# Optimization experiments

Hardware: AMD Instinct MI355X
Metric: run time of the kernel (lower is better)

The kernel has to match this reference:

```python
import jax, jax.numpy as jnp
import numpy as np

N_SAMPLE = 256
POS_IOU_THRESH = 0.7
NEG_IOU_THRESH = 0.3
POS_RATIO = 0.5


def _bbox_iou(bbox_a, bbox_b):
    # bbox_a: [K,4], bbox_b: [G,4] in (x1,y1,x2,y2)
    tl = jnp.maximum(bbox_a[:, None, :2], bbox_b[None, :, :2])  # [K,G,2]
    br = jnp.minimum(bbox_a[:, None, 2:], bbox_b[None, :, 2:])  # [K,G,2]
    wh = br - tl
    inter = wh[..., 0] * wh[..., 1] * jnp.all(tl < br, axis=2)  # [K,G]
    area_a = (bbox_a[:, 2] - bbox_a[:, 0]) * (bbox_a[:, 3] - bbox_a[:, 1])
    area_b = (bbox_b[:, 2] - bbox_b[:, 0]) * (bbox_b[:, 3] - bbox_b[:, 1])
    return inter / (area_a[:, None] + area_b[None, :] - inter)


def _bbox2loc(src_bbox, dst_bbox):
    eps = jnp.asarray(np.finfo(np.float32).eps, src_bbox.dtype)
    width = jnp.maximum(src_bbox[:, 2] - src_bbox[:, 0], eps)
    height = jnp.maximum(src_bbox[:, 3] - src_bbox[:, 1], eps)
    ctr_x = src_bbox[:, 0] + 0.5 * (src_bbox[:, 2] - src_bbox[:, 0])
    ctr_y = src_bbox[:, 1] + 0.5 * (src_bbox[:, 3] - src_bbox[:, 1])
    base_w = dst_bbox[:, 2] - dst_bbox[:, 0]
    base_h = dst_bbox[:, 3] - dst_bbox[:, 1]
    base_cx = dst_bbox[:, 0] + 0.5 * base_w
    base_cy = dst_bbox[:, 1] + 0.5 * base_h
    dx = (base_cx - ctr_x) / width
    dy = (base_cy - ctr_y) / height
    dw = jnp.log(base_w / width)
    dh = jnp.log(base_h / height)
    return jnp.stack([dx, dy, dw, dh], axis=1)  # [K,4]


def _masked_rank(mask, priority):
    # rank (0-based, by priority) of each element within the masked subset;
    # elements outside the mask get ranks >= subset size.
    key = jnp.where(mask, priority, jnp.inf)
    order = jnp.argsort(key)
    n = order.shape[0]
    return jnp.zeros((n,), jnp.int32).at[order].set(jnp.arange(n, dtype=jnp.int32))


def _make_boxes(key, n, coord_max, wh_min, wh_max):
    k1, k2 = jax.random.split(key)
    xy = jax.random.uniform(k1, (n, 2), jnp.float32, 0.0, coord_max)
    wh = jax.random.uniform(k2, (n, 2), jnp.float32, wh_min, wh_max)
    return jnp.concatenate([xy, xy + wh], axis=1)  # valid x1<x2, y1<y2


def setup_inputs() -> dict:
    key = jax.random.key(0)
    ka, kb = jax.random.split(key)
    anchor = _make_boxes(ka, 131072, 800.0, 8.0, 256.0)
    bbox = _make_boxes(kb, 256, 800.0, 16.0, 300.0)
    return {"anchor": anchor, "bbox": bbox}


def reference(anchor, bbox):
    K = anchor.shape[0]
    G = bbox.shape[0]
    ious = _bbox_iou(anchor, bbox)  # [K,G]
    argmax_ious = jnp.argmax(ious, axis=1).astype(jnp.int32)  # best gt per anchor
    max_ious = jnp.max(ious, axis=1)
    gt_argmax_ious = jnp.argmax(ious, axis=0)  # best anchor per gt, [G]
    # force each gt's best anchor to be assigned to that gt
    argmax_ious = argmax_ious.at[gt_argmax_ious].set(jnp.arange(G, dtype=jnp.int32))

    label = jnp.full((K,), -1, jnp.int32)
    label = jnp.where(max_ious < NEG_IOU_THRESH, 0, label)
    label = jnp.where(max_ious >= POS_IOU_THRESH, 1, label)
    label = label.at[gt_argmax_ious].set(1)

    # random subsampling of positives / negatives (fixed key, jit-friendly)
    skey = jax.random.key(42)
    k1, k2 = jax.random.split(skey)
    p_pos = jax.random.uniform(k1, (K,))
    p_neg = jax.random.uniform(k2, (K,))

    n_pos = int(POS_RATIO * N_SAMPLE)
    pos_mask = label == 1
    pos_rank = _masked_rank(pos_mask, p_pos)
    label = jnp.where(pos_mask & (pos_rank >= n_pos), -1, label)

    n_neg = N_SAMPLE - jnp.sum(label == 1)
    neg_mask = label == 0
    neg_rank = _masked_rank(neg_mask, p_neg)
    label = jnp.where(neg_mask & (neg_rank >= n_neg), -1, label)

    loc = _bbox2loc(anchor, bbox[argmax_ious])  # [K,4]
    has_pos = jnp.any(label > 0)
    loc = jnp.where(has_pos, loc, jnp.zeros_like(loc))
    return loc, label
```

## Files before the change

### kernel.cpp

```cpp
#include <hip/hip_runtime.h>
#include <stdint.h>

#define K_ANCH 131072
#define G_BOX  256
#define NPOS_TGT 128
#define NSAMPLE 256
#define POS_CAP 8192
#define NEG_CAP 32768

struct TF2 { uint32_t a, b; };

__host__ __device__ constexpr uint32_t rotl32(uint32_t v, int d) {
  return (v << d) | (v >> (32 - d));
}

__host__ __device__ constexpr TF2 threefry(uint32_t k0, uint32_t k1,
                                           uint32_t x0, uint32_t x1) {
  const uint32_t ks0 = k0, ks1 = k1, ks2 = k0 ^ k1 ^ 0x1BD11BDAu;
  const int R0[4] = {13, 15, 26, 6};
  const int R1[4] = {17, 29, 16, 24};
  x0 += ks0; x1 += ks1;
  for (int r = 0; r < 4; ++r) { x0 += x1; x1 = rotl32(x1, R0[r]); x1 ^= x0; }
  x0 += ks1; x1 += ks2 + 1u;
  for (int r = 0; r < 4; ++r) { x0 += x1; x1 = rotl32(x1, R1[r]); x1 ^= x0; }
  x0 += ks2; x1 += ks0 + 2u;
  for (int r = 0; r < 4; ++r) { x0 += x1; x1 = rotl32(x1, R0[r]); x1 ^= x0; }
  x0 += ks0; x1 += ks1 + 3u;
  for (int r = 0; r < 4; ++r) { x0 += x1; x1 = rotl32(x1, R1[r]); x1 ^= x0; }
  x0 += ks1; x1 += ks2 + 4u;
  for (int r = 0; r < 4; ++r) { x0 += x1; x1 = rotl32(x1, R0[r]); x1 ^= x0; }
  x0 += ks2; x1 += ks0 + 5u;
  return TF2{x0, x1};
}

constexpr TF2 KPOS = threefry(0u, 42u, 0u, 0u);
constexpr TF2 KNEG = threefry(0u, 42u, 0u, 1u);

__device__ __forceinline__ uint32_t rbits(TF2 k, uint32_t i) {
  TF2 r = threefry(k.a, k.b, 0u, i);
  return r.a ^ r.b;
}

__device__ __forceinline__ float p_from_bits(uint32_t bits) {
  uint32_t fb = 0x3f800000u | (bits >> 9);
  float f = __uint_as_float(fb) - 1.0f;
  return fmaxf(f, 0.0f);
}

__device__ __forceinline__ uint64_t prio_key(float p, uint32_t idx) {
  return ((uint64_t)__float_as_uint(p) << 32) | (uint64_t)idx;
}

__device__ __forceinline__ float iou_one(float4 a, float4 b) {
  #pragma clang fp contract(off)
  float tlx = fmaxf(a.x, b.x), tly = fmaxf(a.y, b.y);
  float brx = fminf(a.z, b.z), bry = fminf(a.w, b.w);
  float w = brx - tlx, h = bry - tly;
  float flag = (tlx < brx && tly < bry) ? 1.0f : 0.0f;
  float inter = w * h * flag;
  float area_a = (a.z - a.x) * (a.w - a.y);
  float area_b = (b.z - b.x) * (b.w - b.y);
  float u = (area_a + area_b) - inter;
  float r = inter / u;
  return fmaxf(r, 0.0f);
}

__device__ __forceinline__ float iou_area(float4 a, float4 b, float area_a) {
  #pragma clang fp contract(off)
  float tlx = fmaxf(a.x, b.x), tly = fmaxf(a.y, b.y);
  float brx = fminf(a.z, b.z), bry = fminf(a.w, b.w);
  float w = brx - tlx, h = bry - tly;
  float flag = (tlx < brx && tly < bry) ? 1.0f : 0.0f;
  float inter = w * h * flag;
  float area_b = (b.z - b.x) * (b.w - b.y);
  float u = (area_a + area_b) - inter;
  float r = inter / u;
  return fmaxf(r, 0.0f);
}

template <int CTRL, int RMASK>
__device__ __forceinline__ uint32_t dpp_umax(uint32_t x) {
  uint32_t t = (uint32_t)__builtin_amdgcn_update_dpp((int)x, (int)x, CTRL, RMASK, 0xf, false);
  return x > t ? x : t;
}

struct ScalarBlk {
  unsigned long long cutoff[2];
  int B_pos, r_pos, B_neg, r_neg;
  int do_pos, do_neg, pos_kept, pad;
};

__global__ __launch_bounds__(256) void k_fused(const float4* __restrict__ anchor,
                                               const float4* __restrict__ bbox,
                                               int* __restrict__ argmax,
                                               int* __restrict__ label,
                                               unsigned long long* __restrict__ gkey) {
  __shared__ float4 gts[G_BOX];
  __shared__ unsigned long long gkey_l[G_BOX];
  __shared__ uint32_t xbest[256];
  __shared__ int xbidx[256];
  int tid = threadIdx.x;
  int al = tid & 127, half = tid >> 7;
  int abase = blockIdx.x * 128;
  int i = abase + al;

  gts[tid] = bbox[tid];
  gkey_l[tid] = 0ull;
  __syncthreads();

  float4 a = anchor[i];
  float area_a;
  {
    #pragma clang fp contract(off)
    area_a = (a.z - a.x) * (a.w - a.y);
  }
  int wave_a0 = abase + ((tid >> 6) & 1) * 64;
  uint32_t bestbits = 0u; int bidx = 0;
  int gbase = half * 128;

  #pragma unroll 4
  for (int s = 0; s < 128; ++s) {
    int g = gbase + s;
    float4 b = gts[g];
    float v = iou_area(a, b, area_a);
    uint32_t vb = __float_as_uint(v);
    if (vb > bestbits) { bestbits = vb; bidx = g; }
    uint32_t x = vb;
    x = dpp_umax<0x111, 0xf>(x);
    x = dpp_umax<0x112, 0xf>(x);
    x = dpp_umax<0x114, 0xf>(x);
    x = dpp_umax<0x118, 0xf>(x);
    x = dpp_umax<0x142, 0xa>(x);
    x = dpp_umax<0x143, 0xc>(x);
    uint32_t m = (uint32_t)__builtin_amdgcn_readlane((int)x, 63);
    unsigned long long ball = __ballot(vb == m);
    int lane = __ffsll((long long)ball) - 1;
    unsigned long long key =
        ((unsigned long long)m << 32) |
        (unsigned long long)(~(uint32_t)(wave_a0 + lane));
    if ((tid & 63) == 0) atomicMax(&gkey_l[g], key);
  }

  __syncthreads();
  xbest[tid] = bestbits; xbidx[tid] = bidx;
  __syncthreads();
  if (tid < 128) {
    uint32_t ob = xbest[tid + 128]; int og = xbidx[tid + 128];
    if (ob > bestbits) { bestbits = ob; bidx = og; }
    argmax[i] = bidx;
    float best = __uint_as_float(bestbits);
    int lbl = -1;
    if (best < 0.3f) lbl = 0;
    if (best >= 0.7f) lbl = 1;
    label[i] = lbl;
  }
  atomicMax(&gkey[tid], gkey_l[tid]);
}

__global__ void k_force(const unsigned long long* __restrict__ gkey,
                        int* __restrict__ argmax, int* __restrict__ label) {
  __shared__ int ga[G_BOX];
  int tid = threadIdx.x;
  ga[tid] = (int)(~(uint32_t)(gkey[tid] & 0xffffffffull));
  __syncthreads();
  label[ga[tid]] = 1;
  if (tid == 0) {
    for (int t = 0; t < G_BOX; ++t) argmax[ga[t]] = t;
  }
}

__global__ __launch_bounds__(256) void k_hist(const int* __restrict__ label,
                                              uint32_t* __restrict__ hist) {
  int i = blockIdx.x * 256 + threadIdx.x;
  int lbl = label[i];
  if (lbl < 0) return;
  TF2 k = (lbl == 1) ? KPOS : KNEG;
  float p = p_from_bits(rbits(k, (uint32_t)i));
  int b = (int)(p * 1024.0f); if (b > 1023) b = 1023;
  atomicAdd((unsigned int*)&hist[(lbl == 1 ? 0 : 1024) + b], 1u);
}

__global__ __launch_bounds__(256) void k_select(const uint32_t* __restrict__ hist,
                                                ScalarBlk* __restrict__ sc) {
  __shared__ uint32_t h[2048];
  for (int t = threadIdx.x; t < 2048; t += 256) h[t] = hist[t];
  __syncthreads();
  if (threadIdx.x != 0) return;
  uint32_t total_pos = 0, total_neg = 0;
  for (int b = 0; b < 1024; ++b) total_pos += h[b];
  for (int b = 0; b < 1024; ++b) total_neg += h[1024 + b];
  int pos_kept = total_pos < (uint32_t)NPOS_TGT ? (int)total_pos : NPOS_TGT;
  int n_neg = NSAMPLE - pos_kept;
  sc->pos_kept = pos_kept;
  if (total_pos <= (uint32_t)NPOS_TGT) {
    sc->do_pos = 0; sc->cutoff[0] = ~0ull;
  } else {
    uint32_t cum = 0; int B = 0;
    for (; B < 1024; ++B) { if (cum + h[B] > (uint32_t)NPOS_TGT) break; cum += h[B]; }
    sc->do_pos = 1; sc->B_pos = B; sc->r_pos = NPOS_TGT - (int)cum;
  }
  if (total_neg <= (uint32_t)n_neg) {
    sc->do_neg = 0; sc->cutoff[1] = ~0ull;
  } else {
    uint32_t cum = 0; int B = 0;
    for (; B < 1024; ++B) { if (cum + h[1024 + B] > (uint32_t)n_neg) break; cum += h[1024 + B]; }
    sc->do_neg = 1; sc->B_neg = B; sc->r_neg = n_neg - (int)cum;
  }
}

__global__ __launch_bounds__(256) void k_collect(const int* __restrict__ label,
                                                 uint64_t* __restrict__ pos_list,
                                                 uint64_t* __restrict__ neg_list,
                                                 uint32_t* __restrict__ counters,
                                                 const ScalarBlk* __restrict__ sc) {
  int i = blockIdx.x * 256 + threadIdx.x;
  int lbl = label[i];
  if (lbl < 0) return;
  if (lbl == 1) {
    if (!sc->do_pos) return;
    float p = p_from_bits(rbits(KPOS, (uint32_t)i));
    int b = (int)(p * 1024.0f); if (b > 1023) b = 1023;
    if (b != sc->B_pos) return;
    uint32_t slot = atomicAdd((unsigned int*)&counters[0], 1u);
    if (slot < POS_CAP) pos_list[slot] = prio_key(p, (uint32_t)i);
  } else {
    if (!sc->do_neg) return;
    float p = p_from_bits(rbits(KNEG, (uint32_t)i));
    int b = (int)(p * 1024.0f); if (b > 1023) b = 1023;
    if (b != sc->B_neg) return;
    uint32_t slot = atomicAdd((unsigned int*)&counters[1], 1u);
    if (slot < NEG_CAP) neg_list[slot] = prio_key(p, (uint32_t)i);
  }
}

__global__ __launch_bounds__(256) void k_cutoff(const uint64_t* __restrict__ pos_list,
                                                const uint64_t* __restrict__ neg_list,
                                                const uint32_t* __restrict__ counters,
                                                ScalarBlk* __restrict__ sc) {
  int cls = blockIdx.x;
  int doit = (cls == 0) ? sc->do_pos : sc->do_neg;
  if (!doit) return;
  const uint64_t* list = (cls == 0) ? pos_list : neg_list;
  int cap = (cls == 0) ? POS_CAP : NEG_CAP;
  int m = (int)counters[cls]; if (m > cap) m = cap;
  int r = (cls == 0) ? sc->r_pos : sc->r_neg;
  for (int j = threadIdx.x; j < m; j += 256) {
    uint64_t kj = list[j];
    int rank = 0;
    for (int t = 0; t < m; ++t) rank += (list[t] < kj) ? 1 : 0;
    if (rank == r) sc->cutoff[cls] = (unsigned long long)kj;
  }
}

__global__ __launch_bounds__(256) void k_final(const float4* __restrict__ anchor,
                                               const float4* __restrict__ bbox,
                                               const int* __restrict__ argmax,
                                               const int* __restrict__ label,
                                               const ScalarBlk* __restrict__ sc,
                                               float* __restrict__ out) {
  #pragma clang fp contract(off)
  int i = blockIdx.x * 256 + threadIdx.x;
  int lbl = label[i];
  if (lbl == 1) {
    float p = p_from_bits(rbits(KPOS, (uint32_t)i));
    if (prio_key(p, (uint32_t)i) >= sc->cutoff[0]) lbl = -1;
  } else if (lbl == 0) {
    float p = p_from_bits(rbits(KNEG, (uint32_t)i));
    if (prio_key(p, (uint32_t)i) >= sc->cutoff[1]) lbl = -1;
  }
  out[K_ANCH * 4 + i] = (float)lbl;

  float4 a = anchor[i];
  float4 b = bbox[argmax[i]];
  const float eps = 1.1920928955078125e-07f;
  float w  = fmaxf(a.z - a.x, eps);
  float h  = fmaxf(a.w - a.y, eps);
  float cx = a.x + 0.5f * (a.z - a.x);
  float cy = a.y + 0.5f * (a.w - a.y);
  float bw = b.z - b.x, bh = b.w - b.y;
  float bcx = b.x + 0.5f * bw, bcy = b.y + 0.5f * bh;
  float dx = (bcx - cx) / w, dy = (bcy - cy) / h;
  float dw = logf(bw / w), dh = logf(bh / h);
  float4 o;
  if (sc->pos_kept > 0) o = make_float4(dx, dy, dw, dh);
  else o = make_float4(0.f, 0.f, 0.f, 0.f);
  ((float4*)out)[i] = o;
}

extern "C" void kernel_launch(void* const* d_in, const int* in_sizes, int n_in,
                              void* d_out, int out_size, void* d_ws, size_t ws_size,
                              hipStream_t stream) {
  const float4* anchor = (const float4*)d_in[0];
  const float4* bbox   = (const float4*)d_in[1];
  char* ws = (char*)d_ws;

  uint32_t* hist     = (uint32_t*)(ws);
  uint32_t* counters = (uint32_t*)(ws + 8192);
  unsigned long long* gkey = (unsigned long long*)(ws + 8704);
  ScalarBlk* sc      = (ScalarBlk*)(ws + 10752);
  int* argmax        = (int*)(ws + 16384);
  int* label         = (int*)(ws + 16384 + 524288);
  uint64_t* pos_list = (uint64_t*)(ws + 16384 + 1048576);
  uint64_t* neg_list = pos_list + POS_CAP;

  (void)hipMemsetAsync(ws, 0, 10752, stream);
  k_fused  <<<1024, 256, 0, stream>>>(anchor, bbox, argmax, label, gkey);
  k_force  <<<1,    256, 0, stream>>>(gkey, argmax, label);
  k_hist   <<<512,  256, 0, stream>>>(label, hist);
  k_select <<<1,    256, 0, stream>>>(hist, sc);
  k_collect<<<512,  256, 0, stream>>>(label, pos_list, neg_list, counters, sc);
  k_cutoff <<<2,    256, 0, stream>>>(pos_list, neg_list, counters, sc);
  k_final  <<<512,  256, 0, stream>>>(anchor, bbox, argmax, label, sc, (float*)d_out);
}
```

Before: 151.9 us.

## Split GT range four ways per block and spread per-GT argmax atomics across partitions

```diff
diff --git a/kernel.cpp b/kernel.cpp
--- a/kernel.cpp
+++ b/kernel.cpp
@@ -51,33 +51,6 @@
   return ((uint64_t)__float_as_uint(p) << 32) | (uint64_t)idx;
 }
 
-__device__ __forceinline__ float iou_one(float4 a, float4 b) {
-  #pragma clang fp contract(off)
-  float tlx = fmaxf(a.x, b.x), tly = fmaxf(a.y, b.y);
-  float brx = fminf(a.z, b.z), bry = fminf(a.w, b.w);
-  float w = brx - tlx, h = bry - tly;
-  float flag = (tlx < brx && tly < bry) ? 1.0f : 0.0f;
-  float inter = w * h * flag;
-  float area_a = (a.z - a.x) * (a.w - a.y);
-  float area_b = (b.z - b.x) * (b.w - b.y);
-  float u = (area_a + area_b) - inter;
-  float r = inter / u;
-  return fmaxf(r, 0.0f);
-}
-
-__device__ __forceinline__ float iou_area(float4 a, float4 b, float area_a) {
-  #pragma clang fp contract(off)
-  float tlx = fmaxf(a.x, b.x), tly = fmaxf(a.y, b.y);
-  float brx = fminf(a.z, b.z), bry = fminf(a.w, b.w);
-  float w = brx - tlx, h = bry - tly;
-  float flag = (tlx < brx && tly < bry) ? 1.0f : 0.0f;
-  float inter = w * h * flag;
-  float area_b = (b.z - b.x) * (b.w - b.y);
-  float u = (area_a + area_b) - inter;
-  float r = inter / u;
-  return fmaxf(r, 0.0f);
-}
-
 template <int CTRL, int RMASK>
 __device__ __forceinline__ uint32_t dpp_umax(uint32_t x) {
   uint32_t t = (uint32_t)__builtin_amdgcn_update_dpp((int)x, (int)x, CTRL, RMASK, 0xf, false);
@@ -94,18 +67,22 @@
                                                const float4* __restrict__ bbox,
                                                int* __restrict__ argmax,
                                                int* __restrict__ label,
-                                               unsigned long long* __restrict__ gkey) {
+                                               unsigned long long* __restrict__ gkey_part) {
   __shared__ float4 gts[G_BOX];
-  __shared__ unsigned long long gkey_l[G_BOX];
+  __shared__ float gab[G_BOX];
   __shared__ uint32_t xbest[256];
   __shared__ int xbidx[256];
   int tid = threadIdx.x;
-  int al = tid & 127, half = tid >> 7;
-  int abase = blockIdx.x * 128;
+  int al = tid & 63, q = tid >> 6;
+  int abase = blockIdx.x * 64;
   int i = abase + al;
 
-  gts[tid] = bbox[tid];
-  gkey_l[tid] = 0ull;
+  float4 bb = bbox[tid];
+  gts[tid] = bb;
+  {
+    #pragma clang fp contract(off)
+    gab[tid] = (bb.z - bb.x) * (bb.w - bb.y);
+  }
   __syncthreads();
 
   float4 a = anchor[i];
@@ -114,16 +91,28 @@
     #pragma clang fp contract(off)
     area_a = (a.z - a.x) * (a.w - a.y);
   }
-  int wave_a0 = abase + ((tid >> 6) & 1) * 64;
   uint32_t bestbits = 0u; int bidx = 0;
-  int gbase = half * 128;
-
-  #pragma unroll 4
-  for (int s = 0; s < 128; ++s) {
+  int gbase = q * 64;
+  uint32_t keyhi = 0u, keylo = 0u;
+
+  #pragma unroll 8
+  for (int s = 0; s < 64; ++s) {
     int g = gbase + s;
     float4 b = gts[g];
-    float v = iou_area(a, b, area_a);
-    uint32_t vb = __float_as_uint(v);
+    float ab = gab[g];
+    uint32_t vb;
+    {
+      #pragma clang fp contract(off)
+      float tlx = fmaxf(a.x, b.x), tly = fmaxf(a.y, b.y);
+      float brx = fminf(a.z, b.z), bry = fminf(a.w, b.w);
+      float w = brx - tlx, h = bry - tly;
+      float wh = w * h;
+      bool ok = (tlx < brx) && (tly < bry);
+      float inter = ok ? wh : 0.0f;
+      float u = (area_a + ab) - inter;
+      float v = inter / u;
+      vb = __float_as_uint(v);
+    }
     if (vb > bestbits) { bestbits = vb; bidx = g; }
     uint32_t x = vb;
     x = dpp_umax<0x111, 0xf>(x);
@@ -135,18 +124,25 @@
     uint32_t m = (uint32_t)__builtin_amdgcn_readlane((int)x, 63);
     unsigned long long ball = __ballot(vb == m);
     int lane = __ffsll((long long)ball) - 1;
-    unsigned long long key =
-        ((unsigned long long)m << 32) |
-        (unsigned long long)(~(uint32_t)(wave_a0 + lane));
-    if ((tid & 63) == 0) atomicMax(&gkey_l[g], key);
-  }
-
-  __syncthreads();
+    uint32_t klo = ~(uint32_t)(abase + lane);
+    bool mine = (al == s);
+    keyhi = mine ? m : keyhi;
+    keylo = mine ? klo : keylo;
+  }
+
+  {
+    unsigned long long key = ((unsigned long long)keyhi << 32) | (unsigned long long)keylo;
+    atomicMax(&gkey_part[(blockIdx.x & 7) * G_BOX + gbase + al], key);
+  }
+
   xbest[tid] = bestbits; xbidx[tid] = bidx;
   __syncthreads();
-  if (tid < 128) {
-    uint32_t ob = xbest[tid + 128]; int og = xbidx[tid + 128];
-    if (ob > bestbits) { bestbits = ob; bidx = og; }
+  if (tid < 64) {
+    #pragma unroll
+    for (int qq = 1; qq < 4; ++qq) {
+      uint32_t ob = xbest[qq * 64 + tid]; int og = xbidx[qq * 64 + tid];
+      if (ob > bestbits) { bestbits = ob; bidx = og; }
+    }
     argmax[i] = bidx;
     float best = __uint_as_float(bestbits);
     int lbl = -1;
@@ -154,14 +150,19 @@
     if (best >= 0.7f) lbl = 1;
     label[i] = lbl;
   }
-  atomicMax(&gkey[tid], gkey_l[tid]);
-}
-
-__global__ void k_force(const unsigned long long* __restrict__ gkey,
+}
+
+__global__ void k_force(const unsigned long long* __restrict__ gkey_part,
                         int* __restrict__ argmax, int* __restrict__ label) {
   __shared__ int ga[G_BOX];
   int tid = threadIdx.x;
-  ga[tid] = (int)(~(uint32_t)(gkey[tid] & 0xffffffffull));
+  unsigned long long best = gkey_part[tid];
+  #pragma unroll
+  for (int p = 1; p < 8; ++p) {
+    unsigned long long o = gkey_part[p * G_BOX + tid];
+    if (o > best) best = o;
+  }
+  ga[tid] = (int)(~(uint32_t)(best & 0xffffffffull));
   __syncthreads();
   label[ga[tid]] = 1;
   if (tid == 0) {
@@ -296,16 +297,16 @@
 
   uint32_t* hist     = (uint32_t*)(ws);
   uint32_t* counters = (uint32_t*)(ws + 8192);
-  unsigned long long* gkey = (unsigned long long*)(ws + 8704);
-  ScalarBlk* sc      = (ScalarBlk*)(ws + 10752);
-  int* argmax        = (int*)(ws + 16384);
-  int* label         = (int*)(ws + 16384 + 524288);
-  uint64_t* pos_list = (uint64_t*)(ws + 16384 + 1048576);
+  unsigned long long* gkey_part = (unsigned long long*)(ws + 16384);
+  ScalarBlk* sc      = (ScalarBlk*)(ws + 32768);
+  int* argmax        = (int*)(ws + 65536);
+  int* label         = (int*)(ws + 65536 + 524288);
+  uint64_t* pos_list = (uint64_t*)(ws + 65536 + 1048576);
   uint64_t* neg_list = pos_list + POS_CAP;
 
-  (void)hipMemsetAsync(ws, 0, 10752, stream);
-  k_fused  <<<1024, 256, 0, stream>>>(anchor, bbox, argmax, label, gkey);
-  k_force  <<<1,    256, 0, stream>>>(gkey, argmax, label);
+  (void)hipMemsetAsync(ws, 0, 32768, stream);
+  k_fused  <<<2048, 256, 0, stream>>>(anchor, bbox, argmax, label, gkey_part);
+  k_force  <<<1,    256, 0, stream>>>(gkey_part, argmax, label);
   k_hist   <<<512,  256, 0, stream>>>(label, hist);
   k_select <<<1,    256, 0, stream>>>(hist, sc);
   k_collect<<<512,  256, 0, stream>>>(label, pos_list, neg_list, counters, sc);
```

Result: faster. 143.0 us (-5.9%).
